# Optimization experiments

Hardware: AMD Instinct MI355X
Metric: run time of the kernel (lower is better)

Reference implementation:

```python
import jax, jax.numpy as jnp
import numpy as np

J = 24  # fixed pooling window (SampleLength/N = 1200/50)


def setup_inputs() -> dict:
    key = jax.random.key(0)
    k1, k2, k3 = jax.random.split(key, 3)
    T, N, K, C = 786432, 50, 400, 10  # T = 32768 segments * J
    x = jax.random.normal(k1, (T, N), dtype=jnp.float32)
    W1 = jax.random.normal(k2, (K, N), dtype=jnp.float32) * 0.1
    W2 = jax.random.normal(k3, (C, K), dtype=jnp.float32) * 0.1
    return {"x": x, "W1": W1, "W2": W2}


def reference(x, W1, W2):
    # linear + relu: [T, N] @ [N, K] -> [T, K]
    local_features = jax.nn.relu(jnp.einsum('tn,kn->tk', x, W1))
    # fixed-window mean over consecutive J rows: [T, K] -> [T//J, K]
    T, K = local_features.shape
    features = local_features.reshape(T // J, J, K).mean(axis=1)
    # final linear: [T//J, K] @ [K, C] -> [T//J, C]
    logits = jnp.einsum('bk,ck->bc', features, W2)
    return logits
```

## Files before the change

kernel.cpp:

```cpp
#include <hip/hip_runtime.h>
#include <hip/hip_bf16.h>

#define T_TOTAL 786432
#define N_IN 50
#define K_FEAT 400
#define C_OUT 10
#define NSEG 32768

#define W1F_TASKS (25 * 2 * 64)
#define W2T_OFF_BYTES 51200
#define W2T_FLOATS (25 * 320)
#define W1F32_OFF_BYTES 98304
#define W1F32_TASKS (13 * 4 * 64)
#define W2P_OFF_BYTES 163840
#define W2P_TASKS (13 * 64)
#define PREP_TASKS (W1F_TASKS + W2T_FLOATS + W1F32_TASKS + W2P_TASKS)
#define WS_NEEDED (W2P_OFF_BYTES + (size_t)W2P_TASKS * 8 * 4)

typedef __bf16 bfx8 __attribute__((ext_vector_type(8)));
typedef short  s16x8 __attribute__((ext_vector_type(8)));
typedef float  f32x2 __attribute__((ext_vector_type(2)));
typedef float  f32x4 __attribute__((ext_vector_type(4)));
typedef float  f32x16 __attribute__((ext_vector_type(16)));

static __device__ __forceinline__ short f2bf(float f) {
    union { float f; unsigned u; } v; v.f = f;
    unsigned r = v.u + 0x7fffu + ((v.u >> 16) & 1u);
    return (short)(r >> 16);
}

__global__ void prep_kernel(const float* __restrict__ W1,
                            const float* __restrict__ W2,
                            short* __restrict__ w1f, float* __restrict__ w2t,
                            short* __restrict__ w1f32, float* __restrict__ w2p)
{
    const int gid = blockIdx.x * blockDim.x + threadIdx.x;
    if (gid < W1F_TASKS) {
        const int lane = gid & 63;
        const int s    = (gid >> 6) & 1;
        const int tile = gid >> 7;
        const int m16  = lane & 15;
        const int quad = lane >> 4;
        const float* row = W1 + (tile * 16 + m16) * N_IN;
        s16x8 v;
        #pragma unroll
        for (int j = 0; j < 8; ++j) {
            const int n = s * 32 + quad * 8 + j;
            v[j] = (n < N_IN) ? f2bf(row[n]) : (short)0;
        }
        *(s16x8*)&w1f[gid * 8] = v;
    } else if (gid < W1F_TASKS + W2T_FLOATS) {
        const int i   = gid - W1F_TASKS;
        const int j   = i / 320;
        const int tid = i - j * 320;
        const int o    = tid >> 4;
        const int part = tid & 15;
        const int seg  = (o >= 10) ? 1 : 0;
        const int cls  = o - seg * 10;
        w2t[i] = W2[cls * K_FEAT + part * 25 + j];
    } else if (gid < W1F_TASKS + W2T_FLOATS + W1F32_TASKS) {
        const int i    = gid - W1F_TASKS - W2T_FLOATS;
        const int lane = i & 63;
        const int fi   = i >> 6;
        const int ft   = fi >> 2;
        const int kt   = fi & 3;
        const int feat = ft * 32 + (lane & 31);
        const int cbase = kt * 16 + (lane >> 5) * 8;
        s16x8 v;
        #pragma unroll
        for (int j = 0; j < 8; ++j) {
            const int col = cbase + j;
            v[j] = (feat < K_FEAT && col < N_IN) ? f2bf(W1[feat * N_IN + col])
                                                 : (short)0;
        }
        *(s16x8*)&w1f32[i * 8] = v;
    } else if (gid < PREP_TASKS) {
        const int i    = gid - W1F_TASKS - W2T_FLOATS - W1F32_TASKS;
        const int lane = i & 63;
        const int ft   = i >> 6;
        const int m32  = lane & 31;
        const int h    = lane >> 5;
        const int feat = 32 * ft + m32;
        float v[8];
        #pragma unroll
        for (int c = 0; c < 8; ++c)
            v[c] = (c < 5 && feat < K_FEAT) ? W2[(h * 5 + c) * K_FEAT + feat]
                                            : 0.f;
        float4* dst = (float4*)&w2p[(size_t)i * 8];
        dst[0] = make_float4(v[0], v[1], v[2], v[3]);
        dst[1] = make_float4(v[4], v[5], v[6], v[7]);
    }
}

__global__ __launch_bounds__(256, 3) void phase1_kernel(
    const float* __restrict__ x, const short* __restrict__ w1f32,
    const float* __restrict__ w2p, float* __restrict__ out)
{
    __shared__ __align__(16) short xs[4 * 4800];
    const int tid  = threadIdx.x;
    const int lane = tid & 63;
    const int wv   = tid >> 6;
    const int m32  = lane & 31;
    const int h    = lane >> 5;
    const int chunk = blockIdx.x * 4 + wv;
    short* myxs = xs + wv * 4800;
    const s16x8* wf = (const s16x8*)w1f32;

    s16x8 Bc[4], Bn[4];
    #pragma unroll
    for (int kt = 0; kt < 4; ++kt) Bc[kt] = wf[kt * 64 + lane];

    {
        const float* xg = x + (size_t)chunk * 4800;
        #pragma unroll
        for (int i = 0; i < 19; ++i) {
            const int q = 64 * i + lane;
            if (i < 18 || lane < 48) {
                const float4 v = *(const float4*)(xg + 4 * q);
                int lo, hi;
                asm("v_cvt_pk_bf16_f32 %0, %1, %2" : "=v"(lo) : "v"(v.x), "v"(v.y));
                asm("v_cvt_pk_bf16_f32 %0, %1, %2" : "=v"(hi) : "v"(v.z), "v"(v.w));
                int2 pk; pk.x = lo; pk.y = hi;
                *(int2*)&myxs[4 * q] = pk;
            }
        }
    }
    asm volatile("s_waitcnt lgkmcnt(0)" ::: "memory");
    __builtin_amdgcn_sched_barrier(0);

    s16x8 Af[3][4];
    #pragma unroll
    for (int rt = 0; rt < 3; ++rt) {
        const int row = 32 * rt + m32;
        const short* rp = myxs + row * 50 + 8 * h;
        #pragma unroll
        for (int kt = 0; kt < 3; ++kt) {
            int d0 = *(const int*)(rp + 16 * kt + 0);
            int d1 = *(const int*)(rp + 16 * kt + 2);
            int d2 = *(const int*)(rp + 16 * kt + 4);
            int d3 = *(const int*)(rp + 16 * kt + 6);
            int4 di = {d0, d1, d2, d3};
            Af[rt][kt] = __builtin_bit_cast(s16x8, di);
        }
        int dt = 0;
        if (h == 0) dt = *(const int*)(myxs + row * 50 + 48);
        int4 di3 = {dt, 0, 0, 0};
        Af[rt][3] = __builtin_bit_cast(s16x8, di3);
    }

    const int segbase = chunk * 4;

    float oacc[4][5];
    #pragma unroll
    for (int s = 0; s < 4; ++s)
        #pragma unroll
        for (int c = 0; c < 5; ++c) oacc[s][c] = 0.f;

    f32x16 zacc;
    #pragma unroll
    for (int r = 0; r < 16; ++r) zacc[r] = 0.f;
    const f32x2 z2 = {0.f, 0.f};

    for (int ft = 0; ft < 13; ++ft) {
        const int ftn = (ft < 12) ? ft + 1 : 12;
        #pragma unroll
        for (int kt = 0; kt < 4; ++kt) Bn[kt] = wf[(ftn * 4 + kt) * 64 + lane];
        const float* wl = w2p + (size_t)(ft * 64 + lane) * 8;
        const float4 wa = *(const float4*)wl;
        const float  w4 = wl[4];

        float s0 = 0.f, s1 = 0.f, s2 = 0.f, s3 = 0.f;
        #pragma unroll
        for (int rt = 0; rt < 3; ++rt) {
            f32x16 acc = __builtin_amdgcn_mfma_f32_32x32x16_bf16(
                        __builtin_bit_cast(bfx8, Af[rt][0]),
                        __builtin_bit_cast(bfx8, Bc[0]), zacc, 0, 0, 0);
            #pragma unroll
            for (int kt = 1; kt < 4; ++kt)
                acc = __builtin_amdgcn_mfma_f32_32x32x16_bf16(
                        __builtin_bit_cast(bfx8, Af[rt][kt]),
                        __builtin_bit_cast(bfx8, Bc[kt]), acc, 0, 0, 0);
            f32x2 cv0 = z2, cv1 = z2;
            #pragma unroll
            for (int p = 0; p < 8; ++p) {
                f32x2 v2; v2[0] = acc[2 * p]; v2[1] = acc[2 * p + 1];
                v2 = __builtin_elementwise_max(v2, z2);
                if ((p >> 1) < 3 - rt) cv0 += v2; else cv1 += v2;
            }
            const float c0 = cv0[0] + cv0[1];
            const float c1 = cv1[0] + cv1[1];
            if (rt == 0)      { s0 += c0; s1 += c1; }
            else if (rt == 1) { s1 += c0; s2 += c1; }
            else              { s2 += c0; s3 += c1; }
        }
        s0 += __shfl_xor(s0, 32);
        s1 += __shfl_xor(s1, 32);
        s2 += __shfl_xor(s2, 32);
        s3 += __shfl_xor(s3, 32);

        {
            const float wc[5] = {wa.x, wa.y, wa.z, wa.w, w4};
            const float sv[4] = {s0, s1, s2, s3};
            #pragma unroll
            for (int s = 0; s < 4; ++s)
                #pragma unroll
                for (int c = 0; c < 5; ++c)
                    oacc[s][c] = fmaf(sv[s], wc[c], oacc[s][c]);
        }
        #pragma unroll
        for (int kt = 0; kt < 4; ++kt) Bc[kt] = Bn[kt];
    }

    #pragma unroll
    for (int s = 0; s < 4; ++s)
        #pragma unroll
        for (int c = 0; c < 5; ++c) {
            float v = oacc[s][c];
            v += __shfl_xor(v, 1);
            v += __shfl_xor(v, 2);
            v += __shfl_xor(v, 4);
            v += __shfl_xor(v, 8);
            v += __shfl_xor(v, 16);
            oacc[s][c] = v;
        }
    if (m32 == 0) {
        #pragma unroll
        for (int s = 0; s < 4; ++s)
            #pragma unroll
            for (int c = 0; c < 5; ++c)
                out[(size_t)(segbase + s) * C_OUT + h * 5 + c] =
                    oacc[s][c] * (1.0f / 24.0f);
    }
}

#define FB_CPB 4
#define FB_NTHREADS 320
#define FB_XS_STRIDE 72
#define FB_XS_ROWS (FB_CPB * 48)

__global__ __launch_bounds__(FB_NTHREADS) void classifier_fb(
    const float* __restrict__ x, const short* __restrict__ w1f,
    const float* __restrict__ w2t, float* __restrict__ out)
{
    __shared__ short xs[FB_XS_ROWS * FB_XS_STRIDE];
    __shared__ float pooled[2 * K_FEAT];

    const int tid  = threadIdx.x;
    const int wave = tid >> 6;
    const int lane = tid & 63;
    const int m16  = lane & 15;
    const int quad = lane >> 4;

    {
        const float* xb = x + (size_t)blockIdx.x * (FB_XS_ROWS * N_IN);
        #pragma unroll
        for (int it = 0; it < (FB_XS_ROWS * 25) / FB_NTHREADS; ++it) {
            const int i = tid + it * FB_NTHREADS;
            const int r = i / 25;
            const int c2 = i - r * 25;
            const float2 v = *(const float2*)(xb + 2 * i);
            const int packed = (unsigned short)f2bf(v.x) |
                               ((unsigned)(unsigned short)f2bf(v.y) << 16);
            *(int*)&xs[r * FB_XS_STRIDE + 2 * c2] = packed;
        }
        for (int i = tid; i < FB_XS_ROWS * 7; i += FB_NTHREADS) {
            const int r = i / 7;
            const int c = 50 + 2 * (i - r * 7);
            *(int*)&xs[r * FB_XS_STRIDE + c] = 0;
        }
    }

    s16x8 bfrag[5][2];
    {
        const s16x8* wf = (const s16x8*)w1f;
        #pragma unroll
        for (int t = 0; t < 5; ++t)
            #pragma unroll
            for (int s = 0; s < 2; ++s)
                bfrag[t][s] = wf[((wave * 5 + t) * 2 + s) * 64 + lane];
    }

    const int o    = tid >> 4;
    const int part = tid & 15;
    const int segO = (o >= 10) ? 1 : 0;
    const int cls  = o - segO * 10;
    float w2r[25];
    #pragma unroll
    for (int j = 0; j < 25; ++j) w2r[j] = w2t[j * FB_NTHREADS + tid];

    __syncthreads();

    for (int ciq = 0; ciq < FB_CPB; ++ciq) {
        s16x8 a[3][2];
        #pragma unroll
        for (int r = 0; r < 3; ++r) {
            const short* arow =
                &xs[(ciq * 48 + r * 16 + m16) * FB_XS_STRIDE + quad * 8];
            a[r][0] = *(const s16x8*)(arow);
            a[r][1] = *(const s16x8*)(arow + 32);
        }
        #pragma unroll
        for (int t = 0; t < 5; ++t) {
            float c0 = 0.f, c1 = 0.f;
            #pragma unroll
            for (int r = 0; r < 3; ++r) {
                f32x4 acc = {0.f, 0.f, 0.f, 0.f};
                acc = __builtin_amdgcn_mfma_f32_16x16x32_bf16(
                        __builtin_bit_cast(bfx8, a[r][0]),
                        __builtin_bit_cast(bfx8, bfrag[t][0]), acc, 0, 0, 0);
                acc = __builtin_amdgcn_mfma_f32_16x16x32_bf16(
                        __builtin_bit_cast(bfx8, a[r][1]),
                        __builtin_bit_cast(bfx8, bfrag[t][1]), acc, 0, 0, 0);
                const float s = fmaxf(acc[0], 0.f) + fmaxf(acc[1], 0.f)
                              + fmaxf(acc[2], 0.f) + fmaxf(acc[3], 0.f);
                if (r * 4 + quad < 6) c0 += s; else c1 += s;
            }
            c0 += __shfl_xor(c0, 16); c0 += __shfl_xor(c0, 32);
            c1 += __shfl_xor(c1, 16); c1 += __shfl_xor(c1, 32);
            if (quad == 0) {
                const int feat = (wave * 5 + t) * 16 + m16;
                pooled[feat] = c0;
                pooled[K_FEAT + feat] = c1;
            }
        }
        __syncthreads();

        float sum = 0.f;
        const float* pv = &pooled[segO * K_FEAT + part * 25];
        #pragma unroll
        for (int j = 0; j < 25; ++j) sum += pv[j] * w2r[j];
        sum += __shfl_down(sum, 8, 16);
        sum += __shfl_down(sum, 4, 16);
        sum += __shfl_down(sum, 2, 16);
        sum += __shfl_down(sum, 1, 16);
        if (part == 0) {
            const int chunk = blockIdx.x * FB_CPB + ciq;
            out[(chunk * 2 + segO) * C_OUT + cls] = sum * (1.0f / 24.0f);
        }
        __syncthreads();
    }
}

extern "C" void kernel_launch(void* const* d_in, const int* in_sizes, int n_in,
                              void* d_out, int out_size, void* d_ws, size_t ws_size,
                              hipStream_t stream) {
    const float* x  = (const float*)d_in[0];
    const float* W1 = (const float*)d_in[1];
    const float* W2 = (const float*)d_in[2];
    float* out = (float*)d_out;

    short* w1f   = (short*)d_ws;
    float* w2t   = (float*)((char*)d_ws + W2T_OFF_BYTES);
    short* w1f32 = (short*)((char*)d_ws + W1F32_OFF_BYTES);
    float* w2p   = (float*)((char*)d_ws + W2P_OFF_BYTES);

    prep_kernel<<<(PREP_TASKS + 255) / 256, 256, 0, stream>>>(W1, W2, w1f, w2t,
                                                              w1f32, w2p);

    if (ws_size >= WS_NEEDED) {
        phase1_kernel<<<2048, 256, 0, stream>>>(x, w1f32, w2p, out);
    } else {
        classifier_fb<<<4096, FB_NTHREADS, 0, stream>>>(x, w1f, w2t, out);
    }
}
```

Measured before the change: 250.9 us.

## Ping-pong W1 fragment buffers, fully unroll feature loop, raise MFMA priority

```diff
diff --git a/kernel.cpp b/kernel.cpp
--- a/kernel.cpp
+++ b/kernel.cpp
@@ -106,9 +106,14 @@
     short* myxs = xs + wv * 4800;
     const s16x8* wf = (const s16x8*)w1f32;
 
-    s16x8 Bc[4], Bn[4];
-    #pragma unroll
-    for (int kt = 0; kt < 4; ++kt) Bc[kt] = wf[kt * 64 + lane];
+    auto loadB = [&](s16x8* B, int ft) {
+        #pragma unroll
+        for (int kt = 0; kt < 4; ++kt) B[kt] = wf[(ft * 4 + kt) * 64 + lane];
+    };
+
+    s16x8 BA[4], BB[4];
+    loadB(BA, 0);
+    loadB(BB, 1);
 
     {
         const float* xg = x + (size_t)chunk * 4800;
@@ -150,21 +155,18 @@
 
     const int segbase = chunk * 4;
 
-    float oacc[4][5];
-    #pragma unroll
-    for (int s = 0; s < 4; ++s)
-        #pragma unroll
-        for (int c = 0; c < 5; ++c) oacc[s][c] = 0.f;
+    f32x2 oaccp[2][5];
+    #pragma unroll
+    for (int g = 0; g < 2; ++g)
+        #pragma unroll
+        for (int k = 0; k < 5; ++k) { oaccp[g][k][0] = 0.f; oaccp[g][k][1] = 0.f; }
 
     f32x16 zacc;
     #pragma unroll
     for (int r = 0; r < 16; ++r) zacc[r] = 0.f;
     const f32x2 z2 = {0.f, 0.f};
 
-    for (int ft = 0; ft < 13; ++ft) {
-        const int ftn = (ft < 12) ? ft + 1 : 12;
-        #pragma unroll
-        for (int kt = 0; kt < 4; ++kt) Bn[kt] = wf[(ftn * 4 + kt) * 64 + lane];
+    auto ft_body = [&](int ft, const s16x8* B) {
         const float* wl = w2p + (size_t)(ft * 64 + lane) * 8;
         const float4 wa = *(const float4*)wl;
         const float  w4 = wl[4];
@@ -172,14 +174,16 @@
         float s0 = 0.f, s1 = 0.f, s2 = 0.f, s3 = 0.f;
         #pragma unroll
         for (int rt = 0; rt < 3; ++rt) {
+            __builtin_amdgcn_s_setprio(1);
             f32x16 acc = __builtin_amdgcn_mfma_f32_32x32x16_bf16(
                         __builtin_bit_cast(bfx8, Af[rt][0]),
-                        __builtin_bit_cast(bfx8, Bc[0]), zacc, 0, 0, 0);
+                        __builtin_bit_cast(bfx8, B[0]), zacc, 0, 0, 0);
             #pragma unroll
             for (int kt = 1; kt < 4; ++kt)
                 acc = __builtin_amdgcn_mfma_f32_32x32x16_bf16(
                         __builtin_bit_cast(bfx8, Af[rt][kt]),
-                        __builtin_bit_cast(bfx8, Bc[kt]), acc, 0, 0, 0);
+                        __builtin_bit_cast(bfx8, B[kt]), acc, 0, 0, 0);
+            __builtin_amdgcn_s_setprio(0);
             f32x2 cv0 = z2, cv1 = z2;
             #pragma unroll
             for (int p = 0; p < 8; ++p) {
@@ -198,38 +202,50 @@
         s2 += __shfl_xor(s2, 32);
         s3 += __shfl_xor(s3, 32);
 
-        {
-            const float wc[5] = {wa.x, wa.y, wa.z, wa.w, w4};
-            const float sv[4] = {s0, s1, s2, s3};
-            #pragma unroll
-            for (int s = 0; s < 4; ++s)
+        const float wc[5] = {wa.x, wa.y, wa.z, wa.w, w4};
+        const f32x2 q01 = {s0, s1};
+        const f32x2 q23 = {s2, s3};
+        #pragma unroll
+        for (int k = 0; k < 5; ++k) {
+            const f32x2 wk = {wc[k], wc[k]};
+            oaccp[0][k] = __builtin_elementwise_fma(q01, wk, oaccp[0][k]);
+            oaccp[1][k] = __builtin_elementwise_fma(q23, wk, oaccp[1][k]);
+        }
+    };
+
+    #pragma unroll
+    for (int t = 0; t < 6; ++t) {
+        ft_body(2 * t, BA);
+        loadB(BA, 2 * t + 2);
+        ft_body(2 * t + 1, BB);
+        if (t < 5) loadB(BB, 2 * t + 3);
+    }
+    ft_body(12, BA);
+
+    float red[2][5][2];
+    #pragma unroll
+    for (int g = 0; g < 2; ++g)
+        #pragma unroll
+        for (int k = 0; k < 5; ++k)
+            #pragma unroll
+            for (int p = 0; p < 2; ++p) {
+                float v = oaccp[g][k][p];
+                v += __shfl_xor(v, 1);
+                v += __shfl_xor(v, 2);
+                v += __shfl_xor(v, 4);
+                v += __shfl_xor(v, 8);
+                v += __shfl_xor(v, 16);
+                red[g][k][p] = v;
+            }
+    if (m32 == 0) {
+        #pragma unroll
+        for (int g = 0; g < 2; ++g)
+            #pragma unroll
+            for (int k = 0; k < 5; ++k)
                 #pragma unroll
-                for (int c = 0; c < 5; ++c)
-                    oacc[s][c] = fmaf(sv[s], wc[c], oacc[s][c]);
-        }
-        #pragma unroll
-        for (int kt = 0; kt < 4; ++kt) Bc[kt] = Bn[kt];
-    }
-
-    #pragma unroll
-    for (int s = 0; s < 4; ++s)
-        #pragma unroll
-        for (int c = 0; c < 5; ++c) {
-            float v = oacc[s][c];
-            v += __shfl_xor(v, 1);
-            v += __shfl_xor(v, 2);
-            v += __shfl_xor(v, 4);
-            v += __shfl_xor(v, 8);
-            v += __shfl_xor(v, 16);
-            oacc[s][c] = v;
-        }
-    if (m32 == 0) {
-        #pragma unroll
-        for (int s = 0; s < 4; ++s)
-            #pragma unroll
-            for (int c = 0; c < 5; ++c)
-                out[(size_t)(segbase + s) * C_OUT + h * 5 + c] =
-                    oacc[s][c] * (1.0f / 24.0f);
+                for (int p = 0; p < 2; ++p)
+                    out[(size_t)(segbase + 2 * g + p) * C_OUT + h * 5 + k] =
+                        red[g][k][p] * (1.0f / 24.0f);
     }
 }
 
```

Result: slower. 321.7 us (+28.2%).
